# Kernel tuning notes

Hardware: AMD Instinct MI355X
Metric: run time of the kernel (lower is better)

## Reference

```python
import math
import jax, jax.numpy as jnp
import numpy as np

NUM_HEAD = 16

def get_slopes(n):
    def pow2(n):
        start = 2 ** (-2 ** (-(math.log2(n) - 3)))
        return [start * start ** i for i in range(n)]
    if math.log2(n).is_integer():
        return pow2(n)
    c = 2 ** math.floor(math.log2(n))
    return pow2(c) + get_slopes(2 * c)[0::2][: n - c]

def setup_inputs() -> dict:
    key = jax.random.key(0)
    ks = jax.random.split(key, 9)
    B, T, C = 2, 2048, 2048
    x = jax.random.normal(ks[0], (B, T, C), dtype=jnp.float32)
    std = 0.02
    Wq = std * jax.random.normal(ks[1], (C, C), dtype=jnp.float32)
    Wk = std * jax.random.normal(ks[2], (C, C), dtype=jnp.float32)
    Wv = std * jax.random.normal(ks[3], (C, C), dtype=jnp.float32)
    Wo = (0.02 / np.sqrt(2 * 24)) * jax.random.normal(ks[4], (C, C), dtype=jnp.float32)
    bq = jnp.zeros((C,), jnp.float32)
    bk = jnp.zeros((C,), jnp.float32)
    bv = jnp.zeros((C,), jnp.float32)
    bo = jnp.zeros((C,), jnp.float32)
    return {"x": x, "Wq": Wq, "bq": bq, "Wk": Wk, "bk": bk,
            "Wv": Wv, "bv": bv, "Wo": Wo, "bo": bo}

def reference(x, Wq, bq, Wk, bk, Wv, bv, Wo, bo):
    B, T, C = x.shape
    H = NUM_HEAD
    D = C // H
    slopes = jnp.asarray(get_slopes(H), dtype=jnp.float32)  # [H]

    def split_heads(y):  # [B,T,C] -> [B,H,T,D]
        return y.reshape(B, T, H, D).transpose(0, 2, 1, 3)

    q = split_heads(x @ Wq + bq)
    k = split_heads(x @ Wk + bk)
    v = split_heads(x @ Wv + bv)

    attn = jnp.einsum("bhqd,bhkd->bhqk", q, k) / jnp.sqrt(jnp.float32(D))
    # ALiBi: bias[h, j] = slopes[h] * (j - (T-1)), broadcast over queries
    alibi = slopes[:, None, None] * (jnp.arange(T, dtype=jnp.float32) - (T - 1))[None, None, :]
    attn = attn + alibi  # [B,H,T,T] + [H,1,T]

    causal = jnp.tril(jnp.ones((T, T), dtype=bool))[None, None]
    attn = jnp.where(causal, attn, jnp.finfo(jnp.float32).min)
    p = jax.nn.softmax(attn, axis=-1)

    o = jnp.einsum("bhqk,bhkd->bhqd", p, v).transpose(0, 2, 1, 3).reshape(B, T, C)
    return o @ Wo + bo
```

## Files before the change

kernel.cpp:

```cpp
#include <hip/hip_runtime.h>
#include <math.h>


typedef unsigned short u16;
using bf16x8 = __attribute__((ext_vector_type(8))) short;
using f32x4  = __attribute__((ext_vector_type(4))) float;

__device__ __forceinline__ u16 f2bf(float f) {
  union { float f; unsigned u; } c; c.f = f;
  unsigned r = c.u + 0x7fffu + ((c.u >> 16) & 1u);
  return (u16)(r >> 16);
}
__device__ __forceinline__ float bf2f(u16 b) {
  union { unsigned u; float f; } c; c.u = ((unsigned)b) << 16; return c.f;
}
__device__ __forceinline__ unsigned cvtpk(float a, float b) {
  unsigned r;
  asm("v_cvt_pk_bf16_f32 %0, %1, %2" : "=v"(r) : "v"(a), "v"(b));
  return r;
}
__device__ __forceinline__ void g2l16(const void* g, void* l) {
  __builtin_amdgcn_global_load_lds(
      (const __attribute__((address_space(1))) void*)g,
      (__attribute__((address_space(3))) void*)l, 16, 0, 0);
}

__device__ __forceinline__ int band_jmin(int s, float slope2) {
  const int idist = (int)(36.0f / slope2);
  const int cut = 64 * s - idist - 31;
  return (cut > 0) ? (cut >> 5) : 0;
}

__global__ __launch_bounds__(256) void split_f32(const float* __restrict__ in,
                                                 u16* __restrict__ hi, int n4) {
  for (int i = blockIdx.x * 256 + threadIdx.x; i < n4; i += gridDim.x * 256) {
    const float4 v = ((const float4*)in)[i];
    ushort4 h;
    h.x = f2bf(v.x); h.y = f2bf(v.y); h.z = f2bf(v.z); h.w = f2bf(v.w);
    ((ushort4*)hi)[i] = h;
  }
}

__global__ __launch_bounds__(256) void tsplit4_f32(
    const float* __restrict__ W0, const float* __restrict__ W1,
    const float* __restrict__ W2, const float* __restrict__ W3,
    u16* __restrict__ D0, u16* __restrict__ D1,
    u16* __restrict__ D2, u16* __restrict__ D3,
    int N, int K, float sc0) {
  __shared__ float tile[64][68];
  const int z = blockIdx.z;
  const float* W = (z == 0) ? W0 : (z == 1) ? W1 : (z == 2) ? W2 : W3;
  u16* Wth = (z == 0) ? D0 : (z == 1) ? D1 : (z == 2) ? D2 : D3;
  const float sc = (z == 0) ? sc0 : 1.f;
  const int tid = threadIdx.x;
  const int k0 = blockIdx.y * 64, n0 = blockIdx.x * 64;
  const int rr = tid >> 4, cc = (tid & 15) * 4;
#pragma unroll
  for (int u = 0; u < 4; ++u) {
    const float4 v = *(const float4*)&W[(size_t)(k0 + rr + 16 * u) * N + n0 + cc];
    tile[rr + 16 * u][cc + 0] = v.x;
    tile[rr + 16 * u][cc + 1] = v.y;
    tile[rr + 16 * u][cc + 2] = v.z;
    tile[rr + 16 * u][cc + 3] = v.w;
  }
  __syncthreads();
#pragma unroll
  for (int u = 0; u < 4; ++u) {
    const int nn = rr + 16 * u;
    ushort4 h;
    h.x = f2bf(tile[cc + 0][nn] * sc);
    h.y = f2bf(tile[cc + 1][nn] * sc);
    h.z = f2bf(tile[cc + 2][nn] * sc);
    h.w = f2bf(tile[cc + 3][nn] * sc);
    *(ushort4*)&Wth[(size_t)(n0 + nn) * K + k0 + cc] = h;
  }
}

template <int MODE>
__global__ __launch_bounds__(512, 4) void gemm256x128(
    const u16* __restrict__ Ah, const u16* __restrict__ Bth,
    const float* __restrict__ bias, const float* __restrict__ bias2,
    float bsc, u16* __restrict__ outH, u16* __restrict__ outH2,
    float* __restrict__ outF, int MM, int NN, int KK) {
  __shared__ u16 LA[3][8192];
  __shared__ u16 LB[3][4096];

  const int tid = threadIdx.x;
  const int wave = tid >> 6, lane = tid & 63;
  const int g = lane >> 4, q15 = lane & 15;
  const int wr = wave >> 1, wc = wave & 1;
  const int m0 = blockIdx.y * 256, n0 = blockIdx.x * 128;
  const int NT = KK >> 5;
  const int sxg = ((g ^ ((q15 >> 1) & 3)) << 4);

  f32x4 acc[4][4];
#pragma unroll
  for (int f = 0; f < 4; ++f)
#pragma unroll
    for (int j = 0; j < 4; ++j) acc[f][j] = (f32x4){0.f, 0.f, 0.f, 0.f};

  auto stageA = [&](int t, int rbuf) {
#pragma unroll
    for (int l = 0; l < 2; ++l) {
      const int ch = l * 512 + tid;
      const int row = ch >> 2, slot = ch & 3;
      const size_t ga = (size_t)(m0 + row) * KK + t * 32 +
                        ((slot ^ ((row >> 1) & 3)) * 8);
      g2l16(Ah + ga, (char*)(LA[rbuf]) + ch * 16);
    }
  };
  auto stageB = [&](int t, int rbuf) {
    const int ch = tid;
    const int row = ch >> 2, slot = ch & 3;
    const size_t gb = (size_t)(n0 + row) * KK + t * 32 +
                      ((slot ^ ((row >> 1) & 3)) * 8);
    g2l16(Bth + gb, (char*)(LB[rbuf]) + ch * 16);
  };

  stageA(0, 0); stageB(0, 0);
  __builtin_amdgcn_sched_barrier(0);
  if (NT > 1) { stageA(1, 1); stageB(1, 1); }
  __builtin_amdgcn_sched_barrier(0);
  if (NT > 1) { asm volatile("s_waitcnt vmcnt(3)" ::: "memory"); }
  else        { asm volatile("s_waitcnt vmcnt(0)" ::: "memory"); }
  __builtin_amdgcn_sched_barrier(0);
  __builtin_amdgcn_s_barrier();

  int rb = 0, rb2 = 2;
  for (int t = 0; t < NT; ++t) {
    const char* baseA = (const char*)(LA[rb]);
    const char* baseB = (const char*)(LB[rb]);

    bf16x8 af[4], bf[4];
#pragma unroll
    for (int f = 0; f < 4; ++f)
      af[f] = *(const bf16x8*)(baseA + (wr * 64 + f * 16 + q15) * 64 + sxg);
#pragma unroll
    for (int j = 0; j < 4; ++j)
      bf[j] = *(const bf16x8*)(baseB + (wc * 64 + j * 16 + q15) * 64 + sxg);
    if (t + 2 < NT) { stageA(t + 2, rb2); stageB(t + 2, rb2); }
    __builtin_amdgcn_sched_barrier(0);
    __builtin_amdgcn_s_barrier();
    asm volatile("s_waitcnt lgkmcnt(0)" ::: "memory");
    __builtin_amdgcn_sched_barrier(0);
    __builtin_amdgcn_s_setprio(1);
#pragma unroll
    for (int f = 0; f < 4; ++f)
#pragma unroll
      for (int j = 0; j < 4; ++j)
        acc[f][j] = __builtin_amdgcn_mfma_f32_16x16x32_bf16(
            af[f], bf[j], acc[f][j], 0, 0, 0);
    __builtin_amdgcn_s_setprio(0);
    if (t + 1 < NT) {
      if (t + 2 < NT) { asm volatile("s_waitcnt vmcnt(3)" ::: "memory"); }
      else            { asm volatile("s_waitcnt vmcnt(0)" ::: "memory"); }
    }
    __builtin_amdgcn_sched_barrier(0);
    __builtin_amdgcn_s_barrier();
    rb  = (rb  == 2) ? 0 : rb  + 1;
    rb2 = (rb2 == 2) ? 0 : rb2 + 1;
  }

#pragma unroll
  for (int f = 0; f < 4; ++f)
#pragma unroll
    for (int j = 0; j < 4; ++j)
#pragma unroll
      for (int r = 0; r < 4; ++r) {
        const int row = m0 + wr * 64 + f * 16 + g * 4 + r;
        const int col = n0 + wc * 64 + j * 16 + q15;
        const float v = acc[f][j][r];
        if (MODE == 0) {
          outF[(size_t)row * NN + col] = v + bias[col] * bsc;
        } else if (MODE == 2) {
          outH[(size_t)row * NN + col] = f2bf(v + bias[row] * bsc);
        } else {
          const int sel = col >> 11;
          const int c2 = col & 2047;
          const float vv = v + (sel ? bias2[c2] : bias[c2] * bsc);
          const int bb = row >> 11, tt = row & 2047;
          const int hh = c2 >> 7, dd = c2 & 127;
          (sel ? outH2 : outH)[(((size_t)bb * 16 + hh) * 2048 + tt) * 128 + dd] =
              f2bf(vv);
        }
      }
}

__global__ __launch_bounds__(128) void attn_splitk(
    const u16* __restrict__ Qh, const u16* __restrict__ Kh,
    const u16* __restrict__ Vth, u16* __restrict__ Oh,
    float* __restrict__ Obuf, float* __restrict__ mArr,
    float* __restrict__ lArr, int T, int NB, int BH) {
  __shared__ u16 KS[3][4096];

  const int tid = threadIdx.x;
  const int wid = tid >> 6, lane = tid & 63;
  const int g = lane >> 4, q15 = lane & 15;
  const int L = blockIdx.x;

  int bh, u;
  if (BH == 32) {
    const int k = L >> 8;
    const int c = L & 255;
    bh = (c + 5 * k) & 31;
    u = k * 8 + (c >> 5);
  } else {
    bh = L / 48;
    u = L % 48;
  }
  int s, half;
  if (u < 16)      { s = u;      half = 2; }
  else if (u < 32) { s = 47 - u; half = 0; }
  else             { s = 63 - u; half = 1; }

  const int b = bh >> 4, h = bh & 15;
  const float slope2 = exp2f(-0.5f * (float)(h + 1)) * 1.44269504f;
  const int jmin = band_jmin(s, slope2);
  const bool loEmpty = (jmin >= s + 1);

  if (half == 0 && loEmpty) return;

  int lo, hi;
  if (half == 2)      { lo = jmin;                hi = 2 * s + 2; }
  else if (half == 0) { lo = jmin;                hi = s + 1; }
  else                { lo = loEmpty ? jmin : (s + 1); hi = 2 * s + 2; }
  const int ns = hi - lo;
  const bool maskable = (half != 0);
  const bool normStore = (half == 2) || (half == 1 && loEmpty);

  const int qw0 = s * 64 + wid * 32;
  const size_t vrow0 = (size_t)h * 128;
  const size_t vcol0 = (size_t)b * T;
  const size_t kbase = (size_t)bh * T;

  bf16x8 qfr[2][4];
#pragma unroll
  for (int qf2 = 0; qf2 < 2; ++qf2) {
    const size_t rb = ((size_t)bh * T + qw0 + qf2 * 16 + q15) * 128;
#pragma unroll
    for (int ks = 0; ks < 4; ++ks)
      qfr[qf2][ks] = *(const bf16x8*)&Qh[rb + ks * 32 + g * 8];
  }

  f32x4 oacc[2][8];
#pragma unroll
  for (int a = 0; a < 2; ++a)
#pragma unroll
    for (int n = 0; n < 8; ++n) oacc[a][n] = (f32x4){0.f, 0.f, 0.f, 0.f};
  float m_st[2] = {-1e5f, -1e5f};
  float l_part[2] = {0.f, 0.f};

  auto stageK = [&](int jt, int bf) {
    const int j0 = jt * 32;
#pragma unroll
    for (int uu = 0; uu < 4; ++uu) {
      const int c = wid * 4 + uu;
      const int row = c * 4 + g;
      const int off = (q15 * 16) ^ ((row & 7) << 4);
      const size_t gb = (kbase + j0 + row) * 128;
      g2l16((const char*)(Kh + gb) + off, (char*)(KS[bf]) + c * 1024);
    }
  };
  auto loadV = [&](int jt, bf16x8 (&vf)[8]) {
    const int j0 = jt * 32;
#pragma unroll
    for (int nf = 0; nf < 8; ++nf)
      vf[nf] = *(const bf16x8*)
          &Vth[(vrow0 + nf * 16 + q15) * (size_t)NB + vcol0 + j0 + g * 8];
  };

  bf16x8 vfA[8], vfB[8];
  __builtin_amdgcn_sched_barrier(0);
  stageK(hi - 1, 0);
  if (ns > 1) stageK(hi - 2, 1);
  __builtin_amdgcn_sched_barrier(0);
  loadV(hi - 1, vfA);
  asm volatile("s_waitcnt vmcnt(8)" ::: "memory");
  __builtin_amdgcn_sched_barrier(0);

  int cur = 0;

  auto ITER = [&](int it, bf16x8 (&vc)[8], bf16x8 (&vn)[8]) {
    const int jt = hi - 1 - it;
    const int j0 = jt * 32;
    __builtin_amdgcn_s_barrier();
    __builtin_amdgcn_sched_barrier(0);

    const bool haveV1 = (it + 1 < ns);
    const bool haveK2 = (it + 2 < ns);
    if (haveV1) loadV(jt - 1, vn);
    if (haveK2) {
      int nb = cur + 2; if (nb >= 3) nb -= 3;
      stageK(jt - 2, nb);
    }
    __builtin_amdgcn_sched_barrier(0);

    f32x4 sacc[2][2];
#pragma unroll
    for (int jf = 0; jf < 2; ++jf)
#pragma unroll
      for (int qf2 = 0; qf2 < 2; ++qf2) sacc[jf][qf2] = (f32x4){0.f, 0.f, 0.f, 0.f};
#pragma unroll
    for (int ks = 0; ks < 4; ++ks) {
      bf16x8 ka[2];
#pragma unroll
      for (int jf = 0; jf < 2; ++jf) {
        const int row = jf * 16 + q15;
        const int off = (row * 256 + ks * 64 + g * 16) ^ ((row & 7) << 4);
        ka[jf] = *(const bf16x8*)((const char*)(KS[cur]) + off);
      }
#pragma unroll
      for (int jf = 0; jf < 2; ++jf)
#pragma unroll
        for (int qf2 = 0; qf2 < 2; ++qf2)
          sacc[jf][qf2] = __builtin_amdgcn_mfma_f32_16x16x32_bf16(
              ka[jf], qfr[qf2][ks], sacc[jf][qf2], 0, 0, 0);
    }

    const float jb2 = (float)(j0 + 4 * g - (T - 1));

    unsigned Fw[2][4];
#pragma unroll
    for (int qf2 = 0; qf2 < 2; ++qf2) {
      const int qg = qw0 + qf2 * 16 + q15;
      float sv[2][4];
      float mt = -1e30f;
#pragma unroll
      for (int jf = 0; jf < 2; ++jf)
#pragma unroll
        for (int r = 0; r < 4; ++r) {
          float x = fmaf(slope2, jb2 + (float)(jf * 16 + r), sacc[jf][qf2][r]);
          if (maskable && it < 2) {
            const int jg = j0 + jf * 16 + 4 * g + r;
            x = (jg > qg) ? -1e30f : x;
          }
          sv[jf][r] = x;
          mt = fmaxf(mt, x);
        }
      if (!__all(mt <= m_st[qf2] + 11.0f)) {
        mt = fmaxf(mt, __shfl_xor(mt, 16));
        mt = fmaxf(mt, __shfl_xor(mt, 32));
        const float mnew = fmaxf(m_st[qf2], mt);
        const float scl = exp2f(m_st[qf2] - mnew);
        l_part[qf2] *= scl;
        m_st[qf2] = mnew;
#pragma unroll
        for (int r = 0; r < 4; ++r) {
          const float sc = __shfl(scl, g * 4 + r);
#pragma unroll
          for (int nf = 0; nf < 8; ++nf) oacc[qf2][nf][r] *= sc;
        }
      }
      float rs = 0.f;
      float p[2][4];
#pragma unroll
      for (int jf = 0; jf < 2; ++jf)
#pragma unroll
        for (int r = 0; r < 4; ++r) {
          p[jf][r] = exp2f(sv[jf][r] - m_st[qf2]);
          rs += p[jf][r];
        }
      l_part[qf2] += rs;
      const unsigned W00 = cvtpk(p[0][0], p[0][1]), W01 = cvtpk(p[0][2], p[0][3]);
      const unsigned W10 = cvtpk(p[1][0], p[1][1]), W11 = cvtpk(p[1][2], p[1][3]);
      const int srcA = q15 + ((g & 1) << 5);
      const int srcB = srcA + 16;
      const unsigned A0 = (unsigned)__shfl((int)W00, srcA);
      const unsigned A1 = (unsigned)__shfl((int)W01, srcA);
      const unsigned B0 = (unsigned)__shfl((int)W00, srcB);
      const unsigned B1 = (unsigned)__shfl((int)W01, srcB);
      const unsigned C0 = (unsigned)__shfl((int)W10, srcA);
      const unsigned C1 = (unsigned)__shfl((int)W11, srcA);
      const unsigned D0 = (unsigned)__shfl((int)W10, srcB);
      const unsigned D1 = (unsigned)__shfl((int)W11, srcB);
      const bool hi2 = g >= 2;
      Fw[qf2][0] = hi2 ? C0 : A0;
      Fw[qf2][1] = hi2 ? C1 : A1;
      Fw[qf2][2] = hi2 ? D0 : B0;
      Fw[qf2][3] = hi2 ? D1 : B1;
    }

    if (haveV1) {
      if (haveK2) { asm volatile("s_waitcnt vmcnt(12)" ::: "memory"); }
      else        { asm volatile("s_waitcnt vmcnt(8)"  ::: "memory"); }
    } else        { asm volatile("s_waitcnt vmcnt(0)"  ::: "memory"); }
    __builtin_amdgcn_sched_barrier(0);

    union { unsigned uu[4]; bf16x8 v; } pa0, pa1;
#pragma unroll
    for (int w = 0; w < 4; ++w) { pa0.uu[w] = Fw[0][w]; pa1.uu[w] = Fw[1][w]; }
#pragma unroll
    for (int nf = 0; nf < 8; ++nf) {
      oacc[0][nf] = __builtin_amdgcn_mfma_f32_16x16x32_bf16(pa0.v, vc[nf], oacc[0][nf], 0, 0, 0);
      oacc[1][nf] = __builtin_amdgcn_mfma_f32_16x16x32_bf16(pa1.v, vc[nf], oacc[1][nf], 0, 0, 0);
    }

    cur = (cur == 2) ? 0 : cur + 1;
  };

  for (int it = 0; it < ns;) {
    ITER(it, vfA, vfB); ++it;
    if (it >= ns) break;
    ITER(it, vfB, vfA); ++it;
  }

  float lrow[2];
#pragma unroll
  for (int qf2 = 0; qf2 < 2; ++qf2) {
    float lr = l_part[qf2];
    lr += __shfl_xor(lr, 16);
    lr += __shfl_xor(lr, 32);
    lrow[qf2] = lr;
  }

  if (normStore) {
#pragma unroll
    for (int qf2 = 0; qf2 < 2; ++qf2) {
      const float inv = 1.0f / lrow[qf2];
#pragma unroll
      for (int r = 0; r < 4; ++r) {
        const float iv = __shfl(inv, g * 4 + r);
        const int qrow = qw0 + qf2 * 16 + g * 4 + r;
        const size_t ob = ((size_t)b * T + qrow) * 2048 + h * 128;
#pragma unroll
        for (int nf = 0; nf < 8; ++nf)
          Oh[ob + nf * 16 + q15] = f2bf(oacc[qf2][nf][r] * iv);
      }
    }
  } else {
    const int sp = s - 16;
    const size_t sbase = ((size_t)(bh * 16 + sp) * 2 + half) * 64;
    if (g == 0) {
#pragma unroll
      for (int qf2 = 0; qf2 < 2; ++qf2) {
        mArr[sbase + wid * 32 + qf2 * 16 + q15] = m_st[qf2];
        lArr[sbase + wid * 32 + qf2 * 16 + q15] = lrow[qf2];
      }
    }
    const size_t obase = sbase * 128;
#pragma unroll
    for (int qf2 = 0; qf2 < 2; ++qf2)
#pragma unroll
      for (int r = 0; r < 4; ++r) {
        const int row = wid * 32 + qf2 * 16 + g * 4 + r;
#pragma unroll
        for (int nf = 0; nf < 8; ++nf)
          Obuf[obase + (size_t)row * 128 + nf * 16 + q15] = oacc[qf2][nf][r];
      }
  }
}

__global__ __launch_bounds__(128) void combine_halves(
    const float* __restrict__ Obuf, const float* __restrict__ mArr,
    const float* __restrict__ lArr, u16* __restrict__ Oh, int T) {
  const int idx = blockIdx.x;
  const int row = idx & 63;
  const int sp = (idx >> 6) & 15;
  const int bh = idx >> 10;
  const int d = threadIdx.x;
  const int s = sp + 16;
  const int b = bh >> 4, h = bh & 15;
  const float slope2 = exp2f(-0.5f * (float)(h + 1)) * 1.44269504f;
  if (band_jmin(s, slope2) >= s + 1) return;
  const size_t sbase = ((size_t)(bh * 16 + sp) * 2) * 64;
  const float m1 = mArr[sbase + row],      l1 = lArr[sbase + row];
  const float m2 = mArr[sbase + 64 + row], l2 = lArr[sbase + 64 + row];
  const float M = fmaxf(m1, m2);
  const float w1 = exp2f(m1 - M), w2 = exp2f(m2 - M);
  const float inv = 1.0f / (l1 * w1 + l2 * w2);
  const size_t ob = sbase * 128;
  const float o1 = Obuf[ob + (size_t)row * 128 + d];
  const float o2 = Obuf[ob + 8192 + (size_t)row * 128 + d];
  const float v = (o1 * w1 + o2 * w2) * inv;
  const int qrow = s * 64 + row;
  Oh[((size_t)b * T + qrow) * 2048 + h * 128 + d] = f2bf(v);
}

#define TM 128
#define BKG 8

template <int QKV>
__global__ __launch_bounds__(256) void gemm_f32(
    const float* __restrict__ A, const float* __restrict__ W,
    const float* __restrict__ bias, float* __restrict__ out,
    int M, int N, int K, int T) {
  __shared__ float As[BKG][TM];
  __shared__ float Bs[BKG][TM];
  const int tid = threadIdx.x;
  const int tx = tid & 15, ty = tid >> 4;
  const int m0 = blockIdx.y * TM, n0 = blockIdx.x * TM;
  float acc[8][8];
#pragma unroll
  for (int i = 0; i < 8; ++i)
#pragma unroll
    for (int j = 0; j < 8; ++j) acc[i][j] = 0.f;
  const int arow = tid >> 1, acol = (tid & 1) * 4;
  const int brow = tid >> 5, bcol = (tid & 31) * 4;
  for (int k0 = 0; k0 < K; k0 += BKG) {
    const float4 av = *(const float4*)&A[(size_t)(m0 + arow) * K + k0 + acol];
    const float4 bv = *(const float4*)&W[(size_t)(k0 + brow) * N + n0 + bcol];
    __syncthreads();
    As[acol + 0][arow] = av.x; As[acol + 1][arow] = av.y;
    As[acol + 2][arow] = av.z; As[acol + 3][arow] = av.w;
    *(float4*)&Bs[brow][bcol] = bv;
    __syncthreads();
#pragma unroll
    for (int kk = 0; kk < BKG; ++kk) {
      const float4 a0 = *(const float4*)&As[kk][ty * 4];
      const float4 a1 = *(const float4*)&As[kk][64 + ty * 4];
      const float4 b0 = *(const float4*)&Bs[kk][tx * 4];
      const float4 b1 = *(const float4*)&Bs[kk][64 + tx * 4];
      const float af[8] = {a0.x, a0.y, a0.z, a0.w, a1.x, a1.y, a1.z, a1.w};
      const float bf[8] = {b0.x, b0.y, b0.z, b0.w, b1.x, b1.y, b1.z, b1.w};
#pragma unroll
      for (int i = 0; i < 8; ++i)
#pragma unroll
        for (int j = 0; j < 8; ++j) acc[i][j] += af[i] * bf[j];
    }
  }
#pragma unroll
  for (int a = 0; a < 2; ++a)
#pragma unroll
    for (int i = 0; i < 4; ++i) {
      const int row = m0 + a * 64 + ty * 4 + i;
      const int bb = row / T, t = row % T;
#pragma unroll
      for (int bj = 0; bj < 2; ++bj) {
        const int col = n0 + bj * 64 + tx * 4;
        float4 r;
        r.x = acc[a * 4 + i][bj * 4 + 0] + bias[col + 0];
        r.y = acc[a * 4 + i][bj * 4 + 1] + bias[col + 1];
        r.z = acc[a * 4 + i][bj * 4 + 2] + bias[col + 2];
        r.w = acc[a * 4 + i][bj * 4 + 3] + bias[col + 3];
        if (QKV) {
          const int hh = col >> 7, dd = col & 127;
          *(float4*)&out[(((size_t)bb * 16 + hh) * T + t) * 128 + dd] = r;
        } else {
          *(float4*)&out[(size_t)row * N + col] = r;
        }
      }
    }
}

#define QT 32
#define KT 32
#define DP 132

__global__ __launch_bounds__(256) void flash_f32(
    const float* __restrict__ Q, const float* __restrict__ K,
    const float* __restrict__ V, float* __restrict__ O, int T) {
  __shared__ float Qs[QT][DP];
  __shared__ float Ks[KT][DP];
  __shared__ float Vs[KT][DP];
  __shared__ float Ps[QT][KT + 1];
  const int tid = threadIdx.x;
  const int jh = tid & 15, ih = tid >> 4;
  const int bh = blockIdx.y;
  const int h = bh & 15;
  const int q0 = blockIdx.x * QT;
  const float slope = exp2f(-0.5f * (float)(h + 1));
  const float rsD = 0.08838834764831845f;
  {
    const float* Qg = Q + ((size_t)bh * T + q0) * 128;
    const int r = tid >> 3, p = tid & 7;
#pragma unroll
    for (int u = 0; u < 4; ++u)
      *(float4*)&Qs[r][(p + 8 * u) * 4] = *(const float4*)&Qg[r * 128 + (p + 8 * u) * 4];
  }
  float m_st[2] = {-1e30f, -1e30f};
  float l_st[2] = {0.f, 0.f};
  float accv[2][8] = {};
  const int ktiles = blockIdx.x + 1;
  for (int kt = 0; kt < ktiles; ++kt) {
    const int j0 = kt * KT;
    const float* Kg = K + ((size_t)bh * T + j0) * 128;
    const float* Vg = V + ((size_t)bh * T + j0) * 128;
    __syncthreads();
    {
      const int r = tid >> 3, p = tid & 7;
#pragma unroll
      for (int u = 0; u < 4; ++u) {
        *(float4*)&Ks[r][(p + 8 * u) * 4] = *(const float4*)&Kg[r * 128 + (p + 8 * u) * 4];
        *(float4*)&Vs[r][(p + 8 * u) * 4] = *(const float4*)&Vg[r * 128 + (p + 8 * u) * 4];
      }
    }
    __syncthreads();
    float s00 = 0.f, s01 = 0.f, s10 = 0.f, s11 = 0.f;
#pragma unroll 8
    for (int d4 = 0; d4 < 32; ++d4) {
      const float4 qa = *(const float4*)&Qs[2 * ih + 0][4 * d4];
      const float4 qb = *(const float4*)&Qs[2 * ih + 1][4 * d4];
      const float4 ka = *(const float4*)&Ks[2 * jh + 0][4 * d4];
      const float4 kb = *(const float4*)&Ks[2 * jh + 1][4 * d4];
      s00 += qa.x * ka.x + qa.y * ka.y + qa.z * ka.z + qa.w * ka.w;
      s01 += qa.x * kb.x + qa.y * kb.y + qa.z * kb.z + qa.w * kb.w;
      s10 += qb.x * ka.x + qb.y * ka.y + qb.z * ka.z + qb.w * ka.w;
      s11 += qb.x * kb.x + qb.y * kb.y + qb.z * kb.z + qb.w * kb.w;
    }
    float sc[2][2] = {{s00, s01}, {s10, s11}};
    float mt[2];
#pragma unroll
    for (int r = 0; r < 2; ++r) {
      const int qg = q0 + 2 * ih + r;
#pragma unroll
      for (int c = 0; c < 2; ++c) {
        const int jg = j0 + 2 * jh + c;
        const float svv = sc[r][c] * rsD + slope * (float)(jg - (T - 1));
        sc[r][c] = (jg > qg) ? -1e30f : svv;
      }
      mt[r] = fmaxf(sc[r][0], sc[r][1]);
    }
#pragma unroll
    for (int m = 1; m < 16; m <<= 1) {
      mt[0] = fmaxf(mt[0], __shfl_xor(mt[0], m));
      mt[1] = fmaxf(mt[1], __shfl_xor(mt[1], m));
    }
#pragma unroll
    for (int r = 0; r < 2; ++r) {
      const float mnew = fmaxf(m_st[r], mt[r]);
      const float scl = (m_st[r] > -1e29f) ? expf(m_st[r] - mnew) : 0.f;
      const float p0 = expf(sc[r][0] - mnew);
      const float p1 = expf(sc[r][1] - mnew);
      float rs = p0 + p1;
#pragma unroll
      for (int m = 1; m < 16; m <<= 1) rs += __shfl_xor(rs, m);
      l_st[r] = l_st[r] * scl + rs;
      m_st[r] = mnew;
#pragma unroll
      for (int d = 0; d < 8; ++d) accv[r][d] *= scl;
      Ps[2 * ih + r][2 * jh + 0] = p0;
      Ps[2 * ih + r][2 * jh + 1] = p1;
    }
    __syncthreads();
#pragma unroll 4
    for (int j = 0; j < KT; ++j) {
      const float p0 = Ps[2 * ih + 0][j];
      const float p1 = Ps[2 * ih + 1][j];
      const float4 v0 = *(const float4*)&Vs[j][8 * jh];
      const float4 v1 = *(const float4*)&Vs[j][8 * jh + 4];
      accv[0][0] += p0 * v0.x; accv[0][1] += p0 * v0.y;
      accv[0][2] += p0 * v0.z; accv[0][3] += p0 * v0.w;
      accv[0][4] += p0 * v1.x; accv[0][5] += p0 * v1.y;
      accv[0][6] += p0 * v1.z; accv[0][7] += p0 * v1.w;
      accv[1][0] += p1 * v0.x; accv[1][1] += p1 * v0.y;
      accv[1][2] += p1 * v0.z; accv[1][3] += p1 * v0.w;
      accv[1][4] += p1 * v1.x; accv[1][5] += p1 * v1.y;
      accv[1][6] += p1 * v1.z; accv[1][7] += p1 * v1.w;
    }
  }
  const int b = bh >> 4;
#pragma unroll
  for (int r = 0; r < 2; ++r) {
    const int qg = q0 + 2 * ih + r;
    const float inv = 1.0f / l_st[r];
    float4 o0, o1;
    o0.x = accv[r][0] * inv; o0.y = accv[r][1] * inv;
    o0.z = accv[r][2] * inv; o0.w = accv[r][3] * inv;
    o1.x = accv[r][4] * inv; o1.y = accv[r][5] * inv;
    o1.z = accv[r][6] * inv; o1.w = accv[r][7] * inv;
    float* dst = O + ((size_t)b * T + qg) * 2048 + h * 128 + 8 * jh;
    *(float4*)&dst[0] = o0;
    *(float4*)&dst[4] = o1;
  }
}

extern "C" void kernel_launch(void* const* d_in, const int* in_sizes, int n_in,
                              void* d_out, int out_size, void* d_ws,
                              size_t ws_size, hipStream_t stream) {
  const float* x  = (const float*)d_in[0];
  const float* Wq = (const float*)d_in[1];
  const float* bq = (const float*)d_in[2];
  const float* Wk = (const float*)d_in[3];
  const float* bk = (const float*)d_in[4];
  const float* Wv = (const float*)d_in[5];
  const float* bv = (const float*)d_in[6];
  const float* Wo = (const float*)d_in[7];
  const float* bo = (const float*)d_in[8];
  float* out = (float*)d_out;

  const int C = 2048, T = 2048, H = 16;
  const int M = in_sizes[0] / C;
  const int B = M / T;
  const int BH = B * H;
  const size_t MC = (size_t)M * C, CC = (size_t)C * C;
  const size_t splitO = (size_t)BH * 16 * 2 * 8192;
  const size_t splitML = (size_t)BH * 16 * 2 * 64;
  const size_t need = (5 * MC + 4 * CC) * sizeof(u16) +
                      (splitO + 2 * splitML) * sizeof(float);

  const float QSC = 0.08838834764831845f * 1.44269504088896f;

  if (ws_size >= need && (M % 256) == 0) {
    u16* p = (u16*)d_ws;
    u16* xh   = p; p += MC;
    u16* wqth = p; p += CC;
    u16* wkth = p; p += CC;
    u16* wvth = p; p += CC;
    u16* woth = p; p += CC;
    u16* qh   = p; p += MC;
    u16* kh   = p; p += MC;
    u16* vth  = p; p += MC;
    u16* oh   = p; p += MC;
    float* Obuf = (float*)p;
    float* mArr = Obuf + splitO;
    float* lArr = mArr + splitML;

    split_f32<<<1024, 256, 0, stream>>>(x, xh, (int)(MC / 4));
    dim3 tg(C / 64, C / 64, 4);
    tsplit4_f32<<<tg, 256, 0, stream>>>(Wq, Wk, Wv, Wo, wqth, wkth, wvth,
                                        woth, C, C, QSC);

    dim3 gqk(2 * C / 128, M / 256);
    gemm256x128<3><<<gqk, 512, 0, stream>>>(xh, wqth, bq, bk, QSC, qh, kh,
                                            nullptr, M, 2 * C, C);
    dim3 gv(M / 128, C / 256);
    gemm256x128<2><<<gv, 512, 0, stream>>>(wvth, xh, bv, nullptr, 1.f, vth,
                                           nullptr, nullptr, C, M, C);

    attn_splitk<<<48 * BH, 128, 0, stream>>>(qh, kh, vth, oh, Obuf, mArr,
                                             lArr, T, M, BH);
    combine_halves<<<BH * 16 * 64, 128, 0, stream>>>(Obuf, mArr, lArr, oh, T);

    dim3 gq(C / 128, M / 256);
    gemm256x128<0><<<gq, 512, 0, stream>>>(oh, woth, bo, nullptr, 1.f,
                                           nullptr, nullptr, out, M, C, C);
  } else {
    float* Qw = (float*)d_ws;
    float* Kw = Qw + MC;
    float* Vw = Kw + MC;
    float* Ow = Vw + MC;
    dim3 ggrid(C / TM, M / TM);
    gemm_f32<1><<<ggrid, 256, 0, stream>>>(x, Wq, bq, Qw, M, C, C, T);
    gemm_f32<1><<<ggrid, 256, 0, stream>>>(x, Wk, bk, Kw, M, C, C, T);
    gemm_f32<1><<<ggrid, 256, 0, stream>>>(x, Wv, bv, Vw, M, C, C, T);
    dim3 fgrid(T / QT, B * H);
    flash_f32<<<fgrid, 256, 0, stream>>>(Qw, Kw, Vw, Ow, T);
    gemm_f32<0><<<ggrid, 256, 0, stream>>>(Ow, Wo, bo, out, M, C, C, T);
  }
}
```

Measured before the change: 292.3 us.

## Process 64-key tiles per attention iteration instead of 32

Doubles the key/value block handled per loop iteration in the split-K ALiBi attention kernel, from 32 to 64 keys. K staging in LDS grows to 64 rows per buffer, V is register-prefetched as two 32-column halves, and the QK and PV MFMA loops are widened. The band cutoff, the split point between the two halves and the causal mask window are recomputed at 64-key granularity, with matching changes in combine_halves. The aim is to halve the barriers and loop overhead per unit of work and give the MFMAs longer runs. In exchange it raises register pressure (double-buffered V fragments plus a wider score accumulator) and LDS use. The coarser band cutoff may compute slightly more keys, and the halves become uneven when s+1 is odd.

After: 307.3 us. +5.1%, slower.

```diff
diff --git a/kernel.cpp b/kernel.cpp
--- a/kernel.cpp
+++ b/kernel.cpp
@@ -25,10 +25,10 @@
       (__attribute__((address_space(3))) void*)l, 16, 0, 0);
 }
 
-__device__ __forceinline__ int band_jmin(int s, float slope2) {
+__device__ __forceinline__ int band_jmin64(int s, float slope2) {
   const int idist = (int)(36.0f / slope2);
-  const int cut = 64 * s - idist - 31;
-  return (cut > 0) ? (cut >> 5) : 0;
+  const int cut = 64 * s - idist - 63;
+  return (cut > 0) ? (cut >> 6) : 0;
 }
 
 __global__ __launch_bounds__(256) void split_f32(const float* __restrict__ in,
@@ -191,7 +191,7 @@
     const u16* __restrict__ Vth, u16* __restrict__ Oh,
     float* __restrict__ Obuf, float* __restrict__ mArr,
     float* __restrict__ lArr, int T, int NB, int BH) {
-  __shared__ u16 KS[3][4096];
+  __shared__ u16 KS[3][8192];
 
   const int tid = threadIdx.x;
   const int wid = tid >> 6, lane = tid & 63;
@@ -215,15 +215,16 @@
 
   const int b = bh >> 4, h = bh & 15;
   const float slope2 = exp2f(-0.5f * (float)(h + 1)) * 1.44269504f;
-  const int jmin = band_jmin(s, slope2);
-  const bool loEmpty = (jmin >= s + 1);
+  const int jmin = band_jmin64(s, slope2);
+  const int mid = (s + 1) >> 1;
+  const bool loEmpty = (jmin >= mid);
 
   if (half == 0 && loEmpty) return;
 
   int lo, hi;
-  if (half == 2)      { lo = jmin;                hi = 2 * s + 2; }
-  else if (half == 0) { lo = jmin;                hi = s + 1; }
-  else                { lo = loEmpty ? jmin : (s + 1); hi = 2 * s + 2; }
+  if (half == 2)      { lo = jmin;                hi = s + 1; }
+  else if (half == 0) { lo = jmin;                hi = mid; }
+  else                { lo = loEmpty ? jmin : mid; hi = s + 1; }
   const int ns = hi - lo;
   const bool maskable = (half != 0);
   const bool normStore = (half == 2) || (half == 1 && loEmpty);
@@ -251,38 +252,42 @@
   float l_part[2] = {0.f, 0.f};
 
   auto stageK = [&](int jt, int bf) {
-    const int j0 = jt * 32;
-#pragma unroll
-    for (int uu = 0; uu < 4; ++uu) {
-      const int c = wid * 4 + uu;
+    const int j0 = jt * 64;
+#pragma unroll
+    for (int uu = 0; uu < 8; ++uu) {
+      const int c = wid * 8 + uu;
       const int row = c * 4 + g;
       const int off = (q15 * 16) ^ ((row & 7) << 4);
       const size_t gb = (kbase + j0 + row) * 128;
       g2l16((const char*)(Kh + gb) + off, (char*)(KS[bf]) + c * 1024);
     }
   };
-  auto loadV = [&](int jt, bf16x8 (&vf)[8]) {
-    const int j0 = jt * 32;
-#pragma unroll
-    for (int nf = 0; nf < 8; ++nf)
-      vf[nf] = *(const bf16x8*)
-          &Vth[(vrow0 + nf * 16 + q15) * (size_t)NB + vcol0 + j0 + g * 8];
+  auto loadV = [&](int jt, bf16x8 (&vf)[2][8]) {
+    const int j0 = jt * 64;
+#pragma unroll
+    for (int hh = 0; hh < 2; ++hh)
+#pragma unroll
+      for (int nf = 0; nf < 8; ++nf)
+        vf[hh][nf] = *(const bf16x8*)
+            &Vth[(vrow0 + nf * 16 + q15) * (size_t)NB + vcol0 + j0 +
+                 hh * 32 + g * 8];
   };
 
-  bf16x8 vfA[8], vfB[8];
+  bf16x8 vfA[2][8], vfB[2][8];
   __builtin_amdgcn_sched_barrier(0);
   stageK(hi - 1, 0);
   if (ns > 1) stageK(hi - 2, 1);
   __builtin_amdgcn_sched_barrier(0);
   loadV(hi - 1, vfA);
-  asm volatile("s_waitcnt vmcnt(8)" ::: "memory");
+  if (ns > 1) { asm volatile("s_waitcnt vmcnt(24)" ::: "memory"); }
+  else        { asm volatile("s_waitcnt vmcnt(16)" ::: "memory"); }
   __builtin_amdgcn_sched_barrier(0);
 
   int cur = 0;
 
-  auto ITER = [&](int it, bf16x8 (&vc)[8], bf16x8 (&vn)[8]) {
+  auto ITER = [&](int it, bf16x8 (&vc)[2][8], bf16x8 (&vn)[2][8]) {
     const int jt = hi - 1 - it;
-    const int j0 = jt * 32;
+    const int j0 = jt * 64;
     __builtin_amdgcn_s_barrier();
     __builtin_amdgcn_sched_barrier(0);
 
@@ -295,22 +300,22 @@
     }
     __builtin_amdgcn_sched_barrier(0);
 
-    f32x4 sacc[2][2];
-#pragma unroll
-    for (int jf = 0; jf < 2; ++jf)
+    f32x4 sacc[4][2];
+#pragma unroll
+    for (int jf = 0; jf < 4; ++jf)
 #pragma unroll
       for (int qf2 = 0; qf2 < 2; ++qf2) sacc[jf][qf2] = (f32x4){0.f, 0.f, 0.f, 0.f};
 #pragma unroll
     for (int ks = 0; ks < 4; ++ks) {
-      bf16x8 ka[2];
-#pragma unroll
-      for (int jf = 0; jf < 2; ++jf) {
+      bf16x8 ka[4];
+#pragma unroll
+      for (int jf = 0; jf < 4; ++jf) {
         const int row = jf * 16 + q15;
         const int off = (row * 256 + ks * 64 + g * 16) ^ ((row & 7) << 4);
         ka[jf] = *(const bf16x8*)((const char*)(KS[cur]) + off);
       }
 #pragma unroll
-      for (int jf = 0; jf < 2; ++jf)
+      for (int jf = 0; jf < 4; ++jf)
 #pragma unroll
         for (int qf2 = 0; qf2 < 2; ++qf2)
           sacc[jf][qf2] = __builtin_amdgcn_mfma_f32_16x16x32_bf16(
@@ -319,18 +324,18 @@
 
     const float jb2 = (float)(j0 + 4 * g - (T - 1));
 
-    unsigned Fw[2][4];
+    unsigned Fw[2][2][4];
 #pragma unroll
     for (int qf2 = 0; qf2 < 2; ++qf2) {
       const int qg = qw0 + qf2 * 16 + q15;
-      float sv[2][4];
+      float sv[4][4];
       float mt = -1e30f;
 #pragma unroll
-      for (int jf = 0; jf < 2; ++jf)
+      for (int jf = 0; jf < 4; ++jf)
 #pragma unroll
         for (int r = 0; r < 4; ++r) {
           float x = fmaf(slope2, jb2 + (float)(jf * 16 + r), sacc[jf][qf2][r]);
-          if (maskable && it < 2) {
+          if (maskable && it < 1) {
             const int jg = j0 + jf * 16 + 4 * g + r;
             x = (jg > qg) ? -1e30f : x;
           }
@@ -352,47 +357,61 @@
         }
       }
       float rs = 0.f;
-      float p[2][4];
-#pragma unroll
-      for (int jf = 0; jf < 2; ++jf)
+      float p[4][4];
+#pragma unroll
+      for (int jf = 0; jf < 4; ++jf)
 #pragma unroll
         for (int r = 0; r < 4; ++r) {
           p[jf][r] = exp2f(sv[jf][r] - m_st[qf2]);
           rs += p[jf][r];
         }
       l_part[qf2] += rs;
-      const unsigned W00 = cvtpk(p[0][0], p[0][1]), W01 = cvtpk(p[0][2], p[0][3]);
-      const unsigned W10 = cvtpk(p[1][0], p[1][1]), W11 = cvtpk(p[1][2], p[1][3]);
       const int srcA = q15 + ((g & 1) << 5);
       const int srcB = srcA + 16;
-      const unsigned A0 = (unsigned)__shfl((int)W00, srcA);
-      const unsigned A1 = (unsigned)__shfl((int)W01, srcA);
-      const unsigned B0 = (unsigned)__shfl((int)W00, srcB);
-      const unsigned B1 = (unsigned)__shfl((int)W01, srcB);
-      const unsigned C0 = (unsigned)__shfl((int)W10, srcA);
-      const unsigned C1 = (unsigned)__shfl((int)W11, srcA);
-      const unsigned D0 = (unsigned)__shfl((int)W10, srcB);
-      const unsigned D1 = (unsigned)__shfl((int)W11, srcB);
       const bool hi2 = g >= 2;
-      Fw[qf2][0] = hi2 ? C0 : A0;
-      Fw[qf2][1] = hi2 ? C1 : A1;
-      Fw[qf2][2] = hi2 ? D0 : B0;
-      Fw[qf2][3] = hi2 ? D1 : B1;
+#pragma unroll
+      for (int hh = 0; hh < 2; ++hh) {
+        const unsigned W00 = cvtpk(p[2 * hh][0], p[2 * hh][1]);
+        const unsigned W01 = cvtpk(p[2 * hh][2], p[2 * hh][3]);
+        const unsigned W10 = cvtpk(p[2 * hh + 1][0], p[2 * hh + 1][1]);
+        const unsigned W11 = cvtpk(p[2 * hh + 1][2], p[2 * hh + 1][3]);
+        const unsigned A0 = (unsigned)__shfl((int)W00, srcA);
+        const unsigned A1 = (unsigned)__shfl((int)W01, srcA);
+        const unsigned B0 = (unsigned)__shfl((int)W00, srcB);
+        const unsigned B1 = (unsigned)__shfl((int)W01, srcB);
+        const unsigned C0 = (unsigned)__shfl((int)W10, srcA);
+        const unsigned C1 = (unsigned)__shfl((int)W11, srcA);
+        const unsigned D0 = (unsigned)__shfl((int)W10, srcB);
+        const unsigned D1 = (unsigned)__shfl((int)W11, srcB);
+        Fw[qf2][hh][0] = hi2 ? C0 : A0;
+        Fw[qf2][hh][1] = hi2 ? C1 : A1;
+        Fw[qf2][hh][2] = hi2 ? D0 : B0;
+        Fw[qf2][hh][3] = hi2 ? D1 : B1;
+      }
     }
 
     if (haveV1) {
-      if (haveK2) { asm volatile("s_waitcnt vmcnt(12)" ::: "memory"); }
-      else        { asm volatile("s_waitcnt vmcnt(8)"  ::: "memory"); }
+      if (haveK2) { asm volatile("s_waitcnt vmcnt(24)" ::: "memory"); }
+      else        { asm volatile("s_waitcnt vmcnt(16)" ::: "memory"); }
     } else        { asm volatile("s_waitcnt vmcnt(0)"  ::: "memory"); }
     __builtin_amdgcn_sched_barrier(0);
 
-    union { unsigned uu[4]; bf16x8 v; } pa0, pa1;
-#pragma unroll
-    for (int w = 0; w < 4; ++w) { pa0.uu[w] = Fw[0][w]; pa1.uu[w] = Fw[1][w]; }
+    union { unsigned uu[4]; bf16x8 v; } pa[2][2];
+#pragma unroll
+    for (int qf2 = 0; qf2 < 2; ++qf2)
+#pragma unroll
+      for (int hh = 0; hh < 2; ++hh)
+#pragma unroll
+        for (int w = 0; w < 4; ++w) pa[qf2][hh].uu[w] = Fw[qf2][hh][w];
 #pragma unroll
     for (int nf = 0; nf < 8; ++nf) {
-      oacc[0][nf] = __builtin_amdgcn_mfma_f32_16x16x32_bf16(pa0.v, vc[nf], oacc[0][nf], 0, 0, 0);
-      oacc[1][nf] = __builtin_amdgcn_mfma_f32_16x16x32_bf16(pa1.v, vc[nf], oacc[1][nf], 0, 0, 0);
+      oacc[0][nf] = __builtin_amdgcn_mfma_f32_16x16x32_bf16(pa[0][0].v, vc[0][nf], oacc[0][nf], 0, 0, 0);
+      oacc[1][nf] = __builtin_amdgcn_mfma_f32_16x16x32_bf16(pa[1][0].v, vc[0][nf], oacc[1][nf], 0, 0, 0);
+    }
+#pragma unroll
+    for (int nf = 0; nf < 8; ++nf) {
+      oacc[0][nf] = __builtin_amdgcn_mfma_f32_16x16x32_bf16(pa[0][1].v, vc[1][nf], oacc[0][nf], 0, 0, 0);
+      oacc[1][nf] = __builtin_amdgcn_mfma_f32_16x16x32_bf16(pa[1][1].v, vc[1][nf], oacc[1][nf], 0, 0, 0);
     }
 
     cur = (cur == 2) ? 0 : cur + 1;
@@ -461,7 +480,7 @@
   const int s = sp + 16;
   const int b = bh >> 4, h = bh & 15;
   const float slope2 = exp2f(-0.5f * (float)(h + 1)) * 1.44269504f;
-  if (band_jmin(s, slope2) >= s + 1) return;
+  if (band_jmin64(s, slope2) >= ((s + 1) >> 1)) return;
   const size_t sbase = ((size_t)(bh * 16 + sp) * 2) * 64;
   const float m1 = mArr[sbase + row],      l1 = lArr[sbase + row];
   const float m2 = mArr[sbase + 64 + row], l2 = lArr[sbase + 64 + row];
```
